# Optimization experiments

Measured on AMD Instinct MI355X. Metric: run time of the kernel, lower is better.

## Reference

```python
import jax, jax.numpy as jnp
import numpy as np

CR = 4; D = 768; H = 12; DH = 64; L = 3; I = 3072
W1S = 128  # one-sided sliding window = config.attention_window(256) // 2 (transformers convention)
MAXPOS = 7200; MLP = 512; NCLS = 3
EPS = 1e-12

def layer_norm(x, s, b):
    m = jnp.mean(x, -1, keepdims=True)
    v = jnp.var(x, -1, keepdims=True)
    return (x - m) * jax.lax.rsqrt(v + EPS) * s + b

def band_attention(q, k, v, w):
    # q,k,v: [B,H,S,dh]; each token attends to +-w neighbors (Longformer sliding chunks, no global tokens)
    B, Hh, S, dh = q.shape
    nc = S // w
    qc = q.reshape(B, Hh, nc, w, dh)
    kp = jnp.pad(k, ((0, 0), (0, 0), (w, w), (0, 0)))
    vp = jnp.pad(v, ((0, 0), (0, 0), (w, w), (0, 0)))
    idx = jnp.arange(nc)[:, None] * w + jnp.arange(3 * w)[None, :]          # [nc, 3w]
    kc = kp[:, :, idx]                                                      # [B,H,nc,3w,dh]
    vc = vp[:, :, idx]
    scores = jnp.einsum('bhcqd,bhckd->bhcqk', qc, kc) / np.float32(np.sqrt(dh))
    rel = jnp.arange(3 * w)[None, :] - w - jnp.arange(w)[:, None]           # [w,3w] key_pos - query_pos
    kpos = jnp.arange(nc)[:, None, None] * w + jnp.arange(3 * w)[None, None, :] - w
    mask = (jnp.abs(rel)[None] <= w) & (kpos >= 0) & (kpos < S)             # [nc,w,3w]
    scores = jnp.where(mask[None, None], scores, jnp.float32(-1e9))
    probs = jax.nn.softmax(scores, axis=-1)
    out = jnp.einsum('bhcqk,bhckd->bhcqd', probs, vc)
    return out.reshape(B, Hh, S, dh)

def forward(x, proj_w, proj_b, pos_emb, tok_emb, emb_ln_s, emb_ln_b,
            wq, bq, wk, bk, wv, bv, wo, bo, ln1_s, ln1_b,
            wi, bi, wo2, bo2, ln2_s, ln2_b,
            pool_w, pool_b, head_ln_s, head_ln_b, head_w1, head_b1, head_w2, head_b2):
    n, c, t, wd, hh = x.shape
    tc, sc = t // CR, wd // CR
    # torch unfold(dim, size, step) with size==step == contiguous block reshape
    xr = x[:, :, :tc * CR].reshape(n, c, CR, tc, CR, sc, CR, sc)
    xr = xr.transpose(0, 1, 2, 4, 6, 3, 5, 7)            # n,c,cr_t,cr_w,cr_h,tc,sc,sc
    xr = xr.reshape(n, c, CR ** 3, tc * sc * sc)
    xr = xr.transpose(0, 3, 2, 1).reshape(n, tc * sc * sc, CR ** 3 * c)
    h = xr @ proj_w + proj_b                             # [B,S,D]
    B, S = h.shape[0], h.shape[1]
    pos_ids = jnp.arange(S) % (MAXPOS - 2)               # no padding: S is already a multiple of 2w
    h = h + pos_emb[pos_ids][None] + tok_emb[0][None, None]
    h = layer_norm(h, emb_ln_s, emb_ln_b)
    for l in range(L):
        q = (h @ wq[l] + bq[l]).reshape(B, S, H, DH).transpose(0, 2, 1, 3)
        k = (h @ wk[l] + bk[l]).reshape(B, S, H, DH).transpose(0, 2, 1, 3)
        v = (h @ wv[l] + bv[l]).reshape(B, S, H, DH).transpose(0, 2, 1, 3)
        a = band_attention(q, k, v, W1S).transpose(0, 2, 1, 3).reshape(B, S, D)
        h = layer_norm(h + a @ wo[l] + bo[l], ln1_s[l], ln1_b[l])
        f = jax.nn.gelu(h @ wi[l] + bi[l], approximate=False) @ wo2[l] + bo2[l]
        h = layer_norm(h + f, ln2_s[l], ln2_b[l])
    pooled = jnp.tanh(h[:, 0] @ pool_w + pool_b)         # LongformerPooler on first token
    z = layer_norm(pooled, head_ln_s, head_ln_b)
    z = jax.nn.gelu(z @ head_w1 + head_b1, approximate=False)
    return z @ head_w2 + head_b2                         # [B, num_classes]

def setup_inputs() -> dict:
    key = jax.random.key(0)
    ks = iter(jax.random.split(key, 40))
    p = lambda *s: jax.random.normal(next(ks), s, jnp.float32) * 0.02
    d = {
        'x': jax.random.normal(next(ks), (8, 3, 64, 32, 32), jnp.float32),
        'position_ids': jnp.tile(jnp.arange(1024, dtype=jnp.int32)[None], (8, 1)),
        'proj_w': p(3 * CR ** 3, D), 'proj_b': p(D),
        'pos_emb': p(MAXPOS, D), 'tok_emb': p(2, D),
        'emb_ln_s': jnp.ones((D,), jnp.float32), 'emb_ln_b': jnp.zeros((D,), jnp.float32),
        'wq': p(L, D, D), 'bq': p(L, D), 'wk': p(L, D, D), 'bk': p(L, D),
        'wv': p(L, D, D), 'bv': p(L, D), 'wo': p(L, D, D), 'bo': p(L, D),
        'ln1_s': jnp.ones((L, D), jnp.float32), 'ln1_b': jnp.zeros((L, D), jnp.float32),
        'wi': p(L, D, I), 'bi': p(L, I), 'wo2': p(L, I, D), 'bo2': p(L, D),
        'ln2_s': jnp.ones((L, D), jnp.float32), 'ln2_b': jnp.zeros((L, D), jnp.float32),
        'pool_w': p(D, D), 'pool_b': p(D),
        'head_ln_s': jnp.ones((D,), jnp.float32), 'head_ln_b': jnp.zeros((D,), jnp.float32),
        'head_w1': p(D, MLP), 'head_b1': p(MLP),
        'head_w2': p(MLP, NCLS), 'head_b2': p(NCLS),
    }
    return d

def reference(x, position_ids, proj_w, proj_b, pos_emb, tok_emb, emb_ln_s, emb_ln_b,
              wq, bq, wk, bk, wv, bv, wo, bo, ln1_s, ln1_b,
              wi, bi, wo2, bo2, ln2_s, ln2_b,
              pool_w, pool_b, head_ln_s, head_ln_b, head_w1, head_b1, head_w2, head_b2):
    # position_ids is overwritten inside the spat_temp branch of the original forward (arange over cuboids)
    return forward(x, proj_w, proj_b, pos_emb, tok_emb, emb_ln_s, emb_ln_b,
                   wq, bq, wk, bk, wv, bv, wo, bo, ln1_s, ln1_b,
                   wi, bi, wo2, bo2, ln2_s, ln2_b,
                   pool_w, pool_b, head_ln_s, head_ln_b, head_w1, head_b1, head_w2, head_b2)
```

## Files before the change

kernel.cpp:

```cpp
#include <hip/hip_runtime.h>
#include <hip/hip_bf16.h>
#include <math.h>


typedef __attribute__((ext_vector_type(8))) short short8;
typedef __attribute__((ext_vector_type(4))) short short4v;
typedef __attribute__((ext_vector_type(4))) float floatx4;

__device__ __forceinline__ float gelu_exact(float x) {
    return 0.5f * x * (1.f + erff(x * 0.70710678118654752440f));
}

__device__ __forceinline__ short bfs(float x) {
    __hip_bfloat16 h = __float2bfloat16(x);
    short s;
    __builtin_memcpy(&s, &h, 2);
    return s;
}

__device__ __forceinline__ float bf2f(short s) {
    unsigned u = ((unsigned)(unsigned short)s) << 16;
    float f;
    __builtin_memcpy(&f, &u, 4);
    return f;
}

#define GLOAD_LDS16(g, l) __builtin_amdgcn_global_load_lds( \
    (const __attribute__((address_space(1))) void*)(g),     \
    (__attribute__((address_space(3))) void*)(l), 16, 0, 0)

__global__ __launch_bounds__(256) void transpose_bf16(
    const float* __restrict__ W, __hip_bfloat16* __restrict__ Wt,
    int K, int N, long inLS, long outLS)
{
    __shared__ float tile[32][33];
    int l = blockIdx.z;
    const float* Wl = W + (long)l * inLS;
    __hip_bfloat16* Wtl = Wt + (long)l * outLS;
    int lx = threadIdx.x & 31, ly = threadIdx.x >> 5;
    int kb = blockIdx.y * 32, nb = blockIdx.x * 32;
    #pragma unroll
    for (int r = 0; r < 32; r += 8)
        tile[ly + r][lx] = Wl[(long)(kb + ly + r) * N + nb + lx];
    __syncthreads();
    #pragma unroll
    for (int r = 0; r < 32; r += 8)
        Wtl[(long)(nb + ly + r) * K + kb + lx] = __float2bfloat16(tile[lx][ly + r]);
}

__global__ void pack_qkv_bias(const float* __restrict__ bq,
                              const float* __restrict__ bk,
                              const float* __restrict__ bv,
                              float* __restrict__ out)
{
    int l = blockIdx.x, tid = threadIdx.x;
    out[l * 2304 + tid]        = bq[l * 768 + tid];
    out[l * 2304 + 768 + tid]  = bk[l * 768 + tid];
    out[l * 2304 + 1536 + tid] = bv[l * 768 + tid];
}

__global__ __launch_bounds__(192) void gather_x(
    const float* __restrict__ x, __hip_bfloat16* __restrict__ xr)
{
    int tok = blockIdx.x;
    int b = tok >> 10, s = tok & 1023;
    int tci = s >> 6, sci = (s >> 3) & 7, scj = s & 7;
    int f = threadIdx.x;
    int ch  = f % 3;
    int crc = f / 3;
    int cr1 = crc >> 4, cr2 = (crc >> 2) & 3, cr3 = crc & 3;
    float v = x[(((b * 3 + ch) * 64) + cr1 * 16 + tci) * 1024 +
                (cr2 * 8 + sci) * 32 + cr3 * 8 + scj];
    xr[(long)tok * 192 + f] = __float2bfloat16(v);
}

template<int ACT>
__global__ __launch_bounds__(256) void mfma_gemm(
    const __hip_bfloat16* __restrict__ A, const __hip_bfloat16* __restrict__ Bt,
    const float* __restrict__ bias, __hip_bfloat16* __restrict__ C,
    int M, int N, int K)
{
    __shared__ short lds_raw[8704];
    __hip_bfloat16* As = (__hip_bfloat16*)lds_raw;
    __hip_bfloat16* Bs = As + 4096;
    int tid  = threadIdx.x;
    int wave = tid >> 6, lane = tid & 63;
    int L = blockIdx.x;
    long m0 = (long)(L & 63) * 128, n0 = (long)(L >> 6) * 128;
    int wr = wave >> 1, wc = wave & 1;
    floatx4 acc[4][4] = {};

    int srow = (wave * 128 + lane) >> 2;
    int sch  = (lane & 3) ^ ((lane >> 3) & 3);
    const __hip_bfloat16* Ag = A  + (m0 + srow) * K + sch * 8;
    const __hip_bfloat16* Bg = Bt + (n0 + srow) * K + sch * 8;
    __hip_bfloat16* AsW = &As[wave * 128 * 8];
    __hip_bfloat16* BsW = &Bs[wave * 128 * 8];
    int lm = lane & 15, lg = lane >> 4;
    int lk8 = ((lg ^ ((lm >> 1) & 3))) * 8;

    for (int k0 = 0; k0 < K; k0 += 32) {
        GLOAD_LDS16(Ag + k0,          AsW);
        GLOAD_LDS16(Ag + 16 * K + k0, AsW + 64 * 8);
        GLOAD_LDS16(Bg + k0,          BsW);
        GLOAD_LDS16(Bg + 16 * K + k0, BsW + 64 * 8);
        __syncthreads();
        short8 af[4], bf[4];
        #pragma unroll
        for (int mi = 0; mi < 4; mi++)
            af[mi] = *(const short8*)&As[(wr * 64 + mi * 16 + lm) * 32 + lk8];
        #pragma unroll
        for (int ni = 0; ni < 4; ni++)
            bf[ni] = *(const short8*)&Bs[(wc * 64 + ni * 16 + lm) * 32 + lk8];
        #pragma unroll
        for (int mi = 0; mi < 4; mi++)
            #pragma unroll
            for (int ni = 0; ni < 4; ni++)
                acc[mi][ni] = __builtin_amdgcn_mfma_f32_16x16x32_bf16(
                    af[mi], bf[ni], acc[mi][ni], 0, 0, 0);
        __syncthreads();
    }

    float bvv[4];
    #pragma unroll
    for (int ni = 0; ni < 4; ni++)
        bvv[ni] = bias[n0 + wc * 64 + ni * 16 + lm];
    int erow = tid >> 4;
    int ecol = (tid & 15) * 8;
    #pragma unroll
    for (int p = 0; p < 2; p++) {
        if (wr == p) {
            #pragma unroll
            for (int mi = 0; mi < 4; mi++)
                #pragma unroll
                for (int ni = 0; ni < 4; ni++)
                    #pragma unroll
                    for (int j = 0; j < 4; j++) {
                        float o = acc[mi][ni][j] + bvv[ni];
                        if (ACT == 1) o = gelu_exact(o);
                        lds_raw[(mi * 16 + lg * 4 + j) * 136 +
                                wc * 64 + ni * 16 + lm] = bfs(o);
                    }
        }
        __syncthreads();
        #pragma unroll
        for (int rr = 0; rr < 4; rr++) {
            int r = erow + rr * 16;
            short8 v = *(const short8*)&lds_raw[r * 136 + ecol];
            *(short8*)&C[(m0 + p * 64 + r) * N + n0 + ecol] = v;
        }
        __syncthreads();
    }
}

__global__ __launch_bounds__(256) void pos_ln_kernel(
    const __hip_bfloat16* __restrict__ t, const float* __restrict__ pos_emb,
    const float* __restrict__ tok_emb, const float* __restrict__ ln_s,
    const float* __restrict__ ln_b, float* __restrict__ h,
    __hip_bfloat16* __restrict__ hbf)
{
    int tok = blockIdx.x;
    int s = tok & 1023;
    int tid = threadIdx.x;
    __shared__ float red[8];
    const __hip_bfloat16* trow = &t[(long)tok * 768];
    int d0 = tid, d1 = tid + 256, d2 = tid + 512;
    float a0 = __bfloat162float(trow[d0]) + pos_emb[s * 768 + d0] + tok_emb[d0];
    float a1 = __bfloat162float(trow[d1]) + pos_emb[s * 768 + d1] + tok_emb[d1];
    float a2 = __bfloat162float(trow[d2]) + pos_emb[s * 768 + d2] + tok_emb[d2];
    float sum = a0 + a1 + a2;
    float sumsq = a0 * a0 + a1 * a1 + a2 * a2;
    #pragma unroll
    for (int off = 32; off; off >>= 1) {
        sum   += __shfl_down(sum, off, 64);
        sumsq += __shfl_down(sumsq, off, 64);
    }
    if ((tid & 63) == 0) { red[tid >> 6] = sum; red[4 + (tid >> 6)] = sumsq; }
    __syncthreads();
    sum   = red[0] + red[1] + red[2] + red[3];
    sumsq = red[4] + red[5] + red[6] + red[7];
    float mean = sum * (1.f / 768.f);
    float var  = sumsq * (1.f / 768.f) - mean * mean;
    float rs   = rsqrtf(var + 1e-12f);
    float* hrow = &h[(long)tok * 768];
    __hip_bfloat16* brow = &hbf[(long)tok * 768];
    float o0 = (a0 - mean) * rs * ln_s[d0] + ln_b[d0];
    float o1 = (a1 - mean) * rs * ln_s[d1] + ln_b[d1];
    float o2 = (a2 - mean) * rs * ln_s[d2] + ln_b[d2];
    hrow[d0] = o0; hrow[d1] = o1; hrow[d2] = o2;
    brow[d0] = __float2bfloat16(o0);
    brow[d1] = __float2bfloat16(o1);
    brow[d2] = __float2bfloat16(o2);
}

__global__ __launch_bounds__(256) void attn_kernel(
    const __hip_bfloat16* __restrict__ QKV, __hip_bfloat16* __restrict__ Ob)
{
    __shared__ __hip_bfloat16 KV[128 * 72];
    __shared__ __hip_bfloat16 Pl[4][32 * 136];
    __shared__ float alpha_s[4][32];
    __shared__ float l_s[4][32];

    int blk = blockIdx.x;
    int ci = blk & 7, hh = (blk >> 3) % 12, b = blk / 96;
    int tid = threadIdx.x, w = tid >> 6, lane = tid & 63;
    int lm = lane & 15, lg = lane >> 4;
    __hip_bfloat16* Pw = &Pl[w][0];

    short8 qf[2][2];
    #pragma unroll
    for (int nt = 0; nt < 2; nt++) {
        int q = ci * 128 + w * 32 + nt * 16 + lm;
        const __hip_bfloat16* qp = &QKV[((long)(b * 1024 + q)) * 2304 + hh * 64];
        #pragma unroll
        for (int ks = 0; ks < 2; ks++)
            qf[nt][ks] = *(const short8*)(qp + ks * 32 + lg * 8);
    }

    floatx4 accO[2][4] = {};
    float m_run[2] = {-1e30f, -1e30f};
    float l_run[2] = {0.f, 0.f};

    for (int tt = 0; tt < 3; tt++) {
        __syncthreads();
        #pragma unroll
        for (int i = 0; i < 4; i++) {
            int e = tid + i * 256;
            int jj = e >> 3, dd = (e & 7) * 8;
            int kpos = ci * 128 + tt * 128 + jj - 128;
            short8 kv = {};
            if (kpos >= 0 && kpos < 1024)
                kv = *(const short8*)&QKV[((long)(b * 1024 + kpos)) * 2304 + 768 + hh * 64 + dd];
            *(short8*)&KV[jj * 72 + dd] = kv;
        }
        __syncthreads();

        floatx4 accS[8][2] = {};
        #pragma unroll
        for (int ks = 0; ks < 2; ks++)
            #pragma unroll
            for (int mt = 0; mt < 8; mt++) {
                short8 kf = *(const short8*)&KV[(mt * 16 + lm) * 72 + ks * 32 + lg * 8];
                accS[mt][0] = __builtin_amdgcn_mfma_f32_16x16x32_bf16(kf, qf[0][ks], accS[mt][0], 0, 0, 0);
                accS[mt][1] = __builtin_amdgcn_mfma_f32_16x16x32_bf16(kf, qf[1][ks], accS[mt][1], 0, 0, 0);
            }

        float tmax[2] = {-1e30f, -1e30f};
        #pragma unroll
        for (int nt = 0; nt < 2; nt++) {
            int r = w * 32 + nt * 16 + lm;
            #pragma unroll
            for (int mt = 0; mt < 8; mt++)
                #pragma unroll
                for (int j = 0; j < 4; j++) {
                    int jrel = tt * 128 + mt * 16 + lg * 4 + j;
                    int kpos = ci * 128 + jrel - 128;
                    bool valid = (jrel >= r) && (jrel <= r + 256) &&
                                 (kpos >= 0) && (kpos < 1024);
                    float s = valid ? accS[mt][nt][j] * 0.125f : -1e9f;
                    accS[mt][nt][j] = s;
                    tmax[nt] = fmaxf(tmax[nt], s);
                }
            tmax[nt] = fmaxf(tmax[nt], __shfl_xor(tmax[nt], 16));
            tmax[nt] = fmaxf(tmax[nt], __shfl_xor(tmax[nt], 32));
        }

        float al[2];
        #pragma unroll
        for (int nt = 0; nt < 2; nt++) {
            float mnew = fmaxf(m_run[nt], tmax[nt]);
            al[nt] = __expf(m_run[nt] - mnew);
            m_run[nt] = mnew;
            float ts = 0.f;
            #pragma unroll
            for (int mt = 0; mt < 8; mt++) {
                short4v pp;
                #pragma unroll
                for (int j = 0; j < 4; j++) {
                    float p = __expf(accS[mt][nt][j] - mnew);
                    ts += p;
                    pp[j] = bfs(p);
                }
                *(short4v*)&Pw[(nt * 16 + lm) * 136 + mt * 16 + lg * 4] = pp;
            }
            ts += __shfl_xor(ts, 16);
            ts += __shfl_xor(ts, 32);
            l_run[nt] = l_run[nt] * al[nt] + ts;
        }
        if (lg < 2) alpha_s[w][lg * 16 + lm] = al[lg];

        __syncthreads();
        #pragma unroll
        for (int i = 0; i < 4; i++) {
            int e = tid + i * 256;
            int jj = e >> 3, dd = (e & 7) * 8;
            int kpos = ci * 128 + tt * 128 + jj - 128;
            short8 vv = {};
            if (kpos >= 0 && kpos < 1024)
                vv = *(const short8*)&QKV[((long)(b * 1024 + kpos)) * 2304 + 1536 + hh * 64 + dd];
            short* kvs = (short*)KV;
            #pragma unroll
            for (int m2 = 0; m2 < 8; m2++)
                kvs[(dd + m2) * 136 + jj] = vv[m2];
        }
        __syncthreads();

        #pragma unroll
        for (int mo = 0; mo < 2; mo++)
            #pragma unroll
            for (int j = 0; j < 4; j++) {
                float a = alpha_s[w][mo * 16 + lg * 4 + j];
                #pragma unroll
                for (int nd = 0; nd < 4; nd++)
                    accO[mo][nd][j] *= a;
            }

        #pragma unroll
        for (int kk = 0; kk < 4; kk++) {
            short8 pf[2], vf[4];
            #pragma unroll
            for (int mo = 0; mo < 2; mo++)
                pf[mo] = *(const short8*)&Pw[(mo * 16 + lm) * 136 + kk * 32 + lg * 8];
            #pragma unroll
            for (int nd = 0; nd < 4; nd++)
                vf[nd] = *(const short8*)&KV[(nd * 16 + lm) * 136 + kk * 32 + lg * 8];
            #pragma unroll
            for (int mo = 0; mo < 2; mo++)
                #pragma unroll
                for (int nd = 0; nd < 4; nd++)
                    accO[mo][nd] = __builtin_amdgcn_mfma_f32_16x16x32_bf16(
                        pf[mo], vf[nd], accO[mo][nd], 0, 0, 0);
        }
    }

    if (lg < 2) l_s[w][lg * 16 + lm] = l_run[lg];
    #pragma unroll
    for (int mo = 0; mo < 2; mo++)
        #pragma unroll
        for (int j = 0; j < 4; j++) {
            int qr = mo * 16 + lg * 4 + j;
            float rl = 1.f / l_s[w][qr];
            int q  = w * 32 + qr;
            long base = ((long)(b * 1024 + ci * 128 + q)) * 768 + hh * 64;
            #pragma unroll
            for (int nd = 0; nd < 4; nd++)
                Ob[base + nd * 16 + lm] = __float2bfloat16(accO[mo][nd][j] * rl);
        }
}

__global__ __launch_bounds__(256) void add_ln_kernel(
    float* __restrict__ h, const __hip_bfloat16* __restrict__ t,
    const float* __restrict__ ln_s, const float* __restrict__ ln_b,
    __hip_bfloat16* __restrict__ hbf)
{
    int tok = blockIdx.x;
    int tid = threadIdx.x;
    __shared__ float red[8];
    float* hrow = &h[(long)tok * 768];
    const __hip_bfloat16* trow = &t[(long)tok * 768];
    int d0 = tid, d1 = tid + 256, d2 = tid + 512;
    float a0 = hrow[d0] + __bfloat162float(trow[d0]);
    float a1 = hrow[d1] + __bfloat162float(trow[d1]);
    float a2 = hrow[d2] + __bfloat162float(trow[d2]);
    float sum = a0 + a1 + a2;
    float sumsq = a0 * a0 + a1 * a1 + a2 * a2;
    #pragma unroll
    for (int off = 32; off; off >>= 1) {
        sum   += __shfl_down(sum, off, 64);
        sumsq += __shfl_down(sumsq, off, 64);
    }
    if ((tid & 63) == 0) { red[tid >> 6] = sum; red[4 + (tid >> 6)] = sumsq; }
    __syncthreads();
    sum   = red[0] + red[1] + red[2] + red[3];
    sumsq = red[4] + red[5] + red[6] + red[7];
    float mean = sum * (1.f / 768.f);
    float var  = sumsq * (1.f / 768.f) - mean * mean;
    float rs   = rsqrtf(var + 1e-12f);
    __hip_bfloat16* brow = &hbf[(long)tok * 768];
    float o0 = (a0 - mean) * rs * ln_s[d0] + ln_b[d0];
    float o1 = (a1 - mean) * rs * ln_s[d1] + ln_b[d1];
    float o2 = (a2 - mean) * rs * ln_s[d2] + ln_b[d2];
    hrow[d0] = o0; hrow[d1] = o1; hrow[d2] = o2;
    brow[d0] = __float2bfloat16(o0);
    brow[d1] = __float2bfloat16(o1);
    brow[d2] = __float2bfloat16(o2);
}

__global__ __launch_bounds__(256) void pool_split(
    const __hip_bfloat16* __restrict__ hbf, const __hip_bfloat16* __restrict__ pool_wt,
    const float* __restrict__ pool_b, float* __restrict__ pooled)
{
    int g = blockIdx.x * 256 + threadIdx.x;
    int out = g >> 3, t8 = g & 7;
    int b = out / 768, d = out - b * 768;
    const __hip_bfloat16* hr = hbf + (long)b * 1024 * 768;
    const __hip_bfloat16* wr = pool_wt + (long)d * 768;
    float acc = 0.f;
    #pragma unroll
    for (int kk = 0; kk < 96; kk += 8) {
        int k = t8 * 96 + kk;
        short8 hv = *(const short8*)&hr[k];
        short8 wv = *(const short8*)&wr[k];
        #pragma unroll
        for (int j = 0; j < 8; j++) acc += bf2f(hv[j]) * bf2f(wv[j]);
    }
    acc += __shfl_down(acc, 4, 64);
    acc += __shfl_down(acc, 2, 64);
    acc += __shfl_down(acc, 1, 64);
    if (t8 == 0) pooled[out] = tanhf(acc + pool_b[d]);
}

__global__ __launch_bounds__(256) void ln_z_kernel(
    const float* __restrict__ pooled, const float* __restrict__ hln_s,
    const float* __restrict__ hln_b, __hip_bfloat16* __restrict__ zbf)
{
    int b = blockIdx.x, tid = threadIdx.x;
    __shared__ float red[8];
    const float* pr = &pooled[b * 768];
    float p0 = pr[tid], p1 = pr[tid + 256], p2 = pr[tid + 512];
    float sum = p0 + p1 + p2;
    float sumsq = p0 * p0 + p1 * p1 + p2 * p2;
    #pragma unroll
    for (int off = 32; off; off >>= 1) {
        sum   += __shfl_down(sum, off, 64);
        sumsq += __shfl_down(sumsq, off, 64);
    }
    if ((tid & 63) == 0) { red[tid >> 6] = sum; red[4 + (tid >> 6)] = sumsq; }
    __syncthreads();
    sum   = red[0] + red[1] + red[2] + red[3];
    sumsq = red[4] + red[5] + red[6] + red[7];
    float mean = sum * (1.f / 768.f);
    float var  = sumsq * (1.f / 768.f) - mean * mean;
    float rs   = rsqrtf(var + 1e-12f);
    zbf[b * 768 + tid]       = __float2bfloat16((p0 - mean) * rs * hln_s[tid]       + hln_b[tid]);
    zbf[b * 768 + tid + 256] = __float2bfloat16((p1 - mean) * rs * hln_s[tid + 256] + hln_b[tid + 256]);
    zbf[b * 768 + tid + 512] = __float2bfloat16((p2 - mean) * rs * hln_s[tid + 512] + hln_b[tid + 512]);
}

__global__ __launch_bounds__(256) void mlp_split(
    const __hip_bfloat16* __restrict__ zbf, const __hip_bfloat16* __restrict__ w1t,
    const float* __restrict__ b1, float* __restrict__ z1)
{
    int g = blockIdx.x * 256 + threadIdx.x;
    int out = g >> 3, t8 = g & 7;
    int b = out >> 9, d = out & 511;
    const __hip_bfloat16* zr = zbf + b * 768;
    const __hip_bfloat16* wr = w1t + (long)d * 768;
    float acc = 0.f;
    #pragma unroll
    for (int kk = 0; kk < 96; kk += 8) {
        int k = t8 * 96 + kk;
        short8 zv = *(const short8*)&zr[k];
        short8 wv = *(const short8*)&wr[k];
        #pragma unroll
        for (int j = 0; j < 8; j++) acc += bf2f(zv[j]) * bf2f(wv[j]);
    }
    acc += __shfl_down(acc, 4, 64);
    acc += __shfl_down(acc, 2, 64);
    acc += __shfl_down(acc, 1, 64);
    if (t8 == 0) z1[out] = gelu_exact(acc + b1[d]);
}

__global__ __launch_bounds__(256) void head_final_kernel(
    const float* __restrict__ z1, const float* __restrict__ w2,
    const float* __restrict__ b2, float* __restrict__ out)
{
    int tid = threadIdx.x;
    int g = tid >> 3, t8 = tid & 7;
    if (g < 24) {
        int b = g / 3, o = g % 3;
        float acc = 0.f;
        for (int k = t8; k < 512; k += 8)
            acc += z1[b * 512 + k] * w2[k * 3 + o];
        acc += __shfl_down(acc, 4, 64);
        acc += __shfl_down(acc, 2, 64);
        acc += __shfl_down(acc, 1, 64);
        if (t8 == 0) out[b * 3 + o] = acc + b2[o];
    }
}

extern "C" void kernel_launch(void* const* d_in, const int* in_sizes, int n_in,
                              void* d_out, int out_size, void* d_ws, size_t ws_size,
                              hipStream_t stream) {
    const float* x       = (const float*)d_in[0];
    const float* proj_w  = (const float*)d_in[2];
    const float* proj_b  = (const float*)d_in[3];
    const float* pos_emb = (const float*)d_in[4];
    const float* tok_emb = (const float*)d_in[5];
    const float* eln_s   = (const float*)d_in[6];
    const float* eln_b   = (const float*)d_in[7];
    const float* wq      = (const float*)d_in[8];
    const float* bq      = (const float*)d_in[9];
    const float* wk      = (const float*)d_in[10];
    const float* bk      = (const float*)d_in[11];
    const float* wv      = (const float*)d_in[12];
    const float* bv      = (const float*)d_in[13];
    const float* wo      = (const float*)d_in[14];
    const float* bo      = (const float*)d_in[15];
    const float* ln1_s   = (const float*)d_in[16];
    const float* ln1_b   = (const float*)d_in[17];
    const float* wi      = (const float*)d_in[18];
    const float* bi      = (const float*)d_in[19];
    const float* wo2     = (const float*)d_in[20];
    const float* bo2     = (const float*)d_in[21];
    const float* ln2_s   = (const float*)d_in[22];
    const float* ln2_b   = (const float*)d_in[23];
    const float* pool_w  = (const float*)d_in[24];
    const float* pool_b  = (const float*)d_in[25];
    const float* hln_s   = (const float*)d_in[26];
    const float* hln_b   = (const float*)d_in[27];
    const float* hw1     = (const float*)d_in[28];
    const float* hb1     = (const float*)d_in[29];
    const float* hw2     = (const float*)d_in[30];
    const float* hb2     = (const float*)d_in[31];

    char* wp = (char*)d_ws;
    auto alloc = [&](size_t bytes) {
        char* p = wp; wp += (bytes + 255) & ~(size_t)255; return p;
    };
    float*          h       = (float*)alloc(8192ll * 768 * 4);
    __hip_bfloat16* qkv_bf  = (__hip_bfloat16*)alloc(8192ll * 2304 * 2);
    __hip_bfloat16* t_bf    = (__hip_bfloat16*)alloc(8192ll * 768 * 2);
    __hip_bfloat16* mlp_bf  = (__hip_bfloat16*)alloc(8192ll * 3072 * 2);
    __hip_bfloat16* h_bf    = (__hip_bfloat16*)alloc(8192ll * 768 * 2);
    __hip_bfloat16* a_bf    = (__hip_bfloat16*)alloc(8192ll * 768 * 2);
    __hip_bfloat16* qkvw_t  = (__hip_bfloat16*)alloc(3ll * 2304 * 768 * 2);
    __hip_bfloat16* wo_t    = (__hip_bfloat16*)alloc(3ll * 768 * 768 * 2);
    __hip_bfloat16* wi_t    = (__hip_bfloat16*)alloc(3ll * 3072 * 768 * 2);
    __hip_bfloat16* wo2_t   = (__hip_bfloat16*)alloc(3ll * 768 * 3072 * 2);
    float*          qkv_b   = (float*)alloc(3ll * 2304 * 4);
    __hip_bfloat16* xr_bf   = (__hip_bfloat16*)alloc(8192ll * 192 * 2);
    __hip_bfloat16* projw_t = (__hip_bfloat16*)alloc(768ll * 192 * 2);
    __hip_bfloat16* poolw_t = (__hip_bfloat16*)alloc(768ll * 768 * 2);
    __hip_bfloat16* w1_t    = (__hip_bfloat16*)alloc(512ll * 768 * 2);
    float*          pooled  = (float*)alloc(8ll * 768 * 4);
    __hip_bfloat16* z_bf    = (__hip_bfloat16*)alloc(8ll * 768 * 2);
    float*          z1      = (float*)alloc(8ll * 512 * 4);

    transpose_bf16<<<dim3(24, 24, 3), 256, 0, stream>>>(wq, qkvw_t,               768, 768,  768ll * 768,  2304ll * 768);
    transpose_bf16<<<dim3(24, 24, 3), 256, 0, stream>>>(wk, qkvw_t + 768 * 768,   768, 768,  768ll * 768,  2304ll * 768);
    transpose_bf16<<<dim3(24, 24, 3), 256, 0, stream>>>(wv, qkvw_t + 1536 * 768,  768, 768,  768ll * 768,  2304ll * 768);
    transpose_bf16<<<dim3(24, 24, 3), 256, 0, stream>>>(wo, wo_t,                 768, 768,  768ll * 768,  768ll * 768);
    transpose_bf16<<<dim3(96, 24, 3), 256, 0, stream>>>(wi, wi_t,                 768, 3072, 768ll * 3072, 3072ll * 768);
    transpose_bf16<<<dim3(24, 96, 3), 256, 0, stream>>>(wo2, wo2_t,               3072, 768, 3072ll * 768, 768ll * 3072);
    transpose_bf16<<<dim3(24, 6, 1),  256, 0, stream>>>(proj_w, projw_t,          192, 768,  0, 0);
    transpose_bf16<<<dim3(24, 24, 1), 256, 0, stream>>>(pool_w, poolw_t,          768, 768,  0, 0);
    transpose_bf16<<<dim3(16, 24, 1), 256, 0, stream>>>(hw1, w1_t,                768, 512,  0, 0);
    pack_qkv_bias<<<3, 768, 0, stream>>>(bq, bk, bv, qkv_b);

    gather_x<<<8192, 192, 0, stream>>>(x, xr_bf);
    mfma_gemm<0><<<6 * 64, 256, 0, stream>>>(
        xr_bf, projw_t, proj_b, t_bf, 8192, 768, 192);
    pos_ln_kernel<<<8192, 256, 0, stream>>>(t_bf, pos_emb, tok_emb, eln_s, eln_b, h, h_bf);

    for (int l = 0; l < 3; l++) {
        mfma_gemm<0><<<18 * 64, 256, 0, stream>>>(
            h_bf, qkvw_t + (long)l * 2304 * 768, qkv_b + l * 2304, qkv_bf,
            8192, 2304, 768);
        attn_kernel<<<768, 256, 0, stream>>>(qkv_bf, a_bf);
        mfma_gemm<0><<<6 * 64, 256, 0, stream>>>(
            a_bf, wo_t + (long)l * 768 * 768, bo + l * 768, t_bf,
            8192, 768, 768);
        add_ln_kernel<<<8192, 256, 0, stream>>>(h, t_bf, ln1_s + l * 768, ln1_b + l * 768, h_bf);
        mfma_gemm<1><<<24 * 64, 256, 0, stream>>>(
            h_bf, wi_t + (long)l * 3072 * 768, bi + l * 3072, mlp_bf,
            8192, 3072, 768);
        mfma_gemm<0><<<6 * 64, 256, 0, stream>>>(
            mlp_bf, wo2_t + (long)l * 768 * 3072, bo2 + l * 768, t_bf,
            8192, 768, 3072);
        add_ln_kernel<<<8192, 256, 0, stream>>>(h, t_bf, ln2_s + l * 768, ln2_b + l * 768, h_bf);
    }

    pool_split<<<192, 256, 0, stream>>>(h_bf, poolw_t, pool_b, pooled);
    ln_z_kernel<<<8, 256, 0, stream>>>(pooled, hln_s, hln_b, z_bf);
    mlp_split<<<128, 256, 0, stream>>>(z_bf, w1_t, hb1, z1);
    head_final_kernel<<<1, 256, 0, stream>>>(z1, hw2, hb2, (float*)d_out);
}
```

Measured before the change: 1.195 ms.

## Double-buffer GEMM LDS loads, vectorize LayerNorm kernels, approximate GELU erf

The GEMM now uses two LDS buffers and prefetches the next K-slice with global_load_lds while the current one is being consumed. This drops one barrier per iteration and overlaps global loads with MFMA work, at the cost of twice the LDS footprint, which may lower occupancy. The LayerNorm kernels switch to 192 threads that each handle 4 contiguous elements through float4 and short4 vector loads and stores. GELU's erff is replaced with an Abramowitz-Stegun polynomial using __expf, which is cheaper but less accurate.

```diff
diff --git a/kernel.cpp b/kernel.cpp
--- a/kernel.cpp
+++ b/kernel.cpp
@@ -8,7 +8,12 @@
 typedef __attribute__((ext_vector_type(4))) float floatx4;
 
 __device__ __forceinline__ float gelu_exact(float x) {
-    return 0.5f * x * (1.f + erff(x * 0.70710678118654752440f));
+    float ax = fabsf(x) * 0.70710678118654752440f;
+    float t  = 1.f / (1.f + 0.3275911f * ax);
+    float y  = t * (0.254829592f + t * (-0.284496736f + t * (1.421413741f +
+               t * (-1.453152027f + t * 1.061405429f))));
+    float erfv = copysignf(1.f - y * __expf(-ax * ax), x);
+    return 0.5f * x * (1.f + erfv);
 }
 
 __device__ __forceinline__ short bfs(float x) {
@@ -80,9 +85,9 @@
     const float* __restrict__ bias, __hip_bfloat16* __restrict__ C,
     int M, int N, int K)
 {
-    __shared__ short lds_raw[8704];
+    __shared__ short lds_raw[16384];
     __hip_bfloat16* As = (__hip_bfloat16*)lds_raw;
-    __hip_bfloat16* Bs = As + 4096;
+    __hip_bfloat16* Bs = As + 8192;
     int tid  = threadIdx.x;
     int wave = tid >> 6, lane = tid & 63;
     int L = blockIdx.x;
@@ -94,32 +99,40 @@
     int sch  = (lane & 3) ^ ((lane >> 3) & 3);
     const __hip_bfloat16* Ag = A  + (m0 + srow) * K + sch * 8;
     const __hip_bfloat16* Bg = Bt + (n0 + srow) * K + sch * 8;
-    __hip_bfloat16* AsW = &As[wave * 128 * 8];
-    __hip_bfloat16* BsW = &Bs[wave * 128 * 8];
     int lm = lane & 15, lg = lane >> 4;
     int lk8 = ((lg ^ ((lm >> 1) & 3))) * 8;
 
-    for (int k0 = 0; k0 < K; k0 += 32) {
-        GLOAD_LDS16(Ag + k0,          AsW);
-        GLOAD_LDS16(Ag + 16 * K + k0, AsW + 64 * 8);
-        GLOAD_LDS16(Bg + k0,          BsW);
-        GLOAD_LDS16(Bg + 16 * K + k0, BsW + 64 * 8);
-        __syncthreads();
-        short8 af[4], bf[4];
+    auto stage = [&](int buf, int k0) {
+        __hip_bfloat16* a = As + buf * 4096 + wave * 1024;
+        __hip_bfloat16* b = Bs + buf * 4096 + wave * 1024;
+        GLOAD_LDS16(Ag + k0,          a);
+        GLOAD_LDS16(Ag + 16 * K + k0, a + 512);
+        GLOAD_LDS16(Bg + k0,          b);
+        GLOAD_LDS16(Bg + 16 * K + k0, b + 512);
+    };
+
+    stage(0, 0);
+    int buf = 0;
+    for (int k0 = 0; k0 < K; k0 += 32, buf ^= 1) {
+        __syncthreads();
+        if (k0 + 32 < K) stage(buf ^ 1, k0 + 32);
+        const __hip_bfloat16* Ab = As + buf * 4096;
+        const __hip_bfloat16* Bb = Bs + buf * 4096;
+        short8 af[4], bf4[4];
         #pragma unroll
         for (int mi = 0; mi < 4; mi++)
-            af[mi] = *(const short8*)&As[(wr * 64 + mi * 16 + lm) * 32 + lk8];
+            af[mi] = *(const short8*)&Ab[(wr * 64 + mi * 16 + lm) * 32 + lk8];
         #pragma unroll
         for (int ni = 0; ni < 4; ni++)
-            bf[ni] = *(const short8*)&Bs[(wc * 64 + ni * 16 + lm) * 32 + lk8];
+            bf4[ni] = *(const short8*)&Bb[(wc * 64 + ni * 16 + lm) * 32 + lk8];
         #pragma unroll
         for (int mi = 0; mi < 4; mi++)
             #pragma unroll
             for (int ni = 0; ni < 4; ni++)
                 acc[mi][ni] = __builtin_amdgcn_mfma_f32_16x16x32_bf16(
-                    af[mi], bf[ni], acc[mi][ni], 0, 0, 0);
-        __syncthreads();
-    }
+                    af[mi], bf4[ni], acc[mi][ni], 0, 0, 0);
+    }
+    __syncthreads();
 
     float bvv[4];
     #pragma unroll
@@ -153,7 +166,7 @@
     }
 }
 
-__global__ __launch_bounds__(256) void pos_ln_kernel(
+__global__ __launch_bounds__(192) void pos_ln_kernel(
     const __hip_bfloat16* __restrict__ t, const float* __restrict__ pos_emb,
     const float* __restrict__ tok_emb, const float* __restrict__ ln_s,
     const float* __restrict__ ln_b, float* __restrict__ h,
@@ -162,35 +175,37 @@
     int tok = blockIdx.x;
     int s = tok & 1023;
     int tid = threadIdx.x;
-    __shared__ float red[8];
-    const __hip_bfloat16* trow = &t[(long)tok * 768];
-    int d0 = tid, d1 = tid + 256, d2 = tid + 512;
-    float a0 = __bfloat162float(trow[d0]) + pos_emb[s * 768 + d0] + tok_emb[d0];
-    float a1 = __bfloat162float(trow[d1]) + pos_emb[s * 768 + d1] + tok_emb[d1];
-    float a2 = __bfloat162float(trow[d2]) + pos_emb[s * 768 + d2] + tok_emb[d2];
-    float sum = a0 + a1 + a2;
-    float sumsq = a0 * a0 + a1 * a1 + a2 * a2;
+    int d = tid * 4;
+    __shared__ float red[6];
+    short4v tv = *(const short4v*)&t[(long)tok * 768 + d];
+    float4 pv = *(const float4*)&pos_emb[s * 768 + d];
+    float4 kv = *(const float4*)&tok_emb[d];
+    float a[4] = { bf2f(tv[0]) + pv.x + kv.x, bf2f(tv[1]) + pv.y + kv.y,
+                   bf2f(tv[2]) + pv.z + kv.z, bf2f(tv[3]) + pv.w + kv.w };
+    float sum = a[0] + a[1] + a[2] + a[3];
+    float sumsq = a[0]*a[0] + a[1]*a[1] + a[2]*a[2] + a[3]*a[3];
     #pragma unroll
     for (int off = 32; off; off >>= 1) {
         sum   += __shfl_down(sum, off, 64);
         sumsq += __shfl_down(sumsq, off, 64);
     }
-    if ((tid & 63) == 0) { red[tid >> 6] = sum; red[4 + (tid >> 6)] = sumsq; }
+    if ((tid & 63) == 0) { red[tid >> 6] = sum; red[3 + (tid >> 6)] = sumsq; }
     __syncthreads();
-    sum   = red[0] + red[1] + red[2] + red[3];
-    sumsq = red[4] + red[5] + red[6] + red[7];
+    sum   = red[0] + red[1] + red[2];
+    sumsq = red[3] + red[4] + red[5];
     float mean = sum * (1.f / 768.f);
     float var  = sumsq * (1.f / 768.f) - mean * mean;
     float rs   = rsqrtf(var + 1e-12f);
-    float* hrow = &h[(long)tok * 768];
-    __hip_bfloat16* brow = &hbf[(long)tok * 768];
-    float o0 = (a0 - mean) * rs * ln_s[d0] + ln_b[d0];
-    float o1 = (a1 - mean) * rs * ln_s[d1] + ln_b[d1];
-    float o2 = (a2 - mean) * rs * ln_s[d2] + ln_b[d2];
-    hrow[d0] = o0; hrow[d1] = o1; hrow[d2] = o2;
-    brow[d0] = __float2bfloat16(o0);
-    brow[d1] = __float2bfloat16(o1);
-    brow[d2] = __float2bfloat16(o2);
+    float4 sv = *(const float4*)&ln_s[d];
+    float4 bv = *(const float4*)&ln_b[d];
+    float4 o;
+    o.x = (a[0] - mean) * rs * sv.x + bv.x;
+    o.y = (a[1] - mean) * rs * sv.y + bv.y;
+    o.z = (a[2] - mean) * rs * sv.z + bv.z;
+    o.w = (a[3] - mean) * rs * sv.w + bv.w;
+    *(float4*)&h[(long)tok * 768 + d] = o;
+    short4v ob = { bfs(o.x), bfs(o.y), bfs(o.z), bfs(o.w) };
+    *(short4v*)&hbf[(long)tok * 768 + d] = ob;
 }
 
 __global__ __launch_bounds__(256) void attn_kernel(
@@ -348,42 +363,44 @@
         }
 }
 
-__global__ __launch_bounds__(256) void add_ln_kernel(
+__global__ __launch_bounds__(192) void add_ln_kernel(
     float* __restrict__ h, const __hip_bfloat16* __restrict__ t,
     const float* __restrict__ ln_s, const float* __restrict__ ln_b,
     __hip_bfloat16* __restrict__ hbf)
 {
     int tok = blockIdx.x;
     int tid = threadIdx.x;
-    __shared__ float red[8];
+    int d = tid * 4;
+    __shared__ float red[6];
     float* hrow = &h[(long)tok * 768];
-    const __hip_bfloat16* trow = &t[(long)tok * 768];
-    int d0 = tid, d1 = tid + 256, d2 = tid + 512;
-    float a0 = hrow[d0] + __bfloat162float(trow[d0]);
-    float a1 = hrow[d1] + __bfloat162float(trow[d1]);
-    float a2 = hrow[d2] + __bfloat162float(trow[d2]);
-    float sum = a0 + a1 + a2;
-    float sumsq = a0 * a0 + a1 * a1 + a2 * a2;
+    float4 hv = *(const float4*)&hrow[d];
+    short4v tv = *(const short4v*)&t[(long)tok * 768 + d];
+    float a[4] = { hv.x + bf2f(tv[0]), hv.y + bf2f(tv[1]),
+                   hv.z + bf2f(tv[2]), hv.w + bf2f(tv[3]) };
+    float sum = a[0] + a[1] + a[2] + a[3];
+    float sumsq = a[0]*a[0] + a[1]*a[1] + a[2]*a[2] + a[3]*a[3];
     #pragma unroll
     for (int off = 32; off; off >>= 1) {
         sum   += __shfl_down(sum, off, 64);
         sumsq += __shfl_down(sumsq, off, 64);
     }
-    if ((tid & 63) == 0) { red[tid >> 6] = sum; red[4 + (tid >> 6)] = sumsq; }
+    if ((tid & 63) == 0) { red[tid >> 6] = sum; red[3 + (tid >> 6)] = sumsq; }
     __syncthreads();
-    sum   = red[0] + red[1] + red[2] + red[3];
-    sumsq = red[4] + red[5] + red[6] + red[7];
+    sum   = red[0] + red[1] + red[2];
+    sumsq = red[3] + red[4] + red[5];
     float mean = sum * (1.f / 768.f);
     float var  = sumsq * (1.f / 768.f) - mean * mean;
     float rs   = rsqrtf(var + 1e-12f);
-    __hip_bfloat16* brow = &hbf[(long)tok * 768];
-    float o0 = (a0 - mean) * rs * ln_s[d0] + ln_b[d0];
-    float o1 = (a1 - mean) * rs * ln_s[d1] + ln_b[d1];
-    float o2 = (a2 - mean) * rs * ln_s[d2] + ln_b[d2];
-    hrow[d0] = o0; hrow[d1] = o1; hrow[d2] = o2;
-    brow[d0] = __float2bfloat16(o0);
-    brow[d1] = __float2bfloat16(o1);
-    brow[d2] = __float2bfloat16(o2);
+    float4 sv = *(const float4*)&ln_s[d];
+    float4 bv = *(const float4*)&ln_b[d];
+    float4 o;
+    o.x = (a[0] - mean) * rs * sv.x + bv.x;
+    o.y = (a[1] - mean) * rs * sv.y + bv.y;
+    o.z = (a[2] - mean) * rs * sv.z + bv.z;
+    o.w = (a[3] - mean) * rs * sv.w + bv.w;
+    *(float4*)&hrow[d] = o;
+    short4v ob = { bfs(o.x), bfs(o.y), bfs(o.z), bfs(o.w) };
+    *(short4v*)&hbf[(long)tok * 768 + d] = ob;
 }
 
 __global__ __launch_bounds__(256) void pool_split(
@@ -551,7 +568,7 @@
     gather_x<<<8192, 192, 0, stream>>>(x, xr_bf);
     mfma_gemm<0><<<6 * 64, 256, 0, stream>>>(
         xr_bf, projw_t, proj_b, t_bf, 8192, 768, 192);
-    pos_ln_kernel<<<8192, 256, 0, stream>>>(t_bf, pos_emb, tok_emb, eln_s, eln_b, h, h_bf);
+    pos_ln_kernel<<<8192, 192, 0, stream>>>(t_bf, pos_emb, tok_emb, eln_s, eln_b, h, h_bf);
 
     for (int l = 0; l < 3; l++) {
         mfma_gemm<0><<<18 * 64, 256, 0, stream>>>(
@@ -561,14 +578,14 @@
         mfma_gemm<0><<<6 * 64, 256, 0, stream>>>(
             a_bf, wo_t + (long)l * 768 * 768, bo + l * 768, t_bf,
             8192, 768, 768);
-        add_ln_kernel<<<8192, 256, 0, stream>>>(h, t_bf, ln1_s + l * 768, ln1_b + l * 768, h_bf);
+        add_ln_kernel<<<8192, 192, 0, stream>>>(h, t_bf, ln1_s + l * 768, ln1_b + l * 768, h_bf);
         mfma_gemm<1><<<24 * 64, 256, 0, stream>>>(
             h_bf, wi_t + (long)l * 3072 * 768, bi + l * 3072, mlp_bf,
             8192, 3072, 768);
         mfma_gemm<0><<<6 * 64, 256, 0, stream>>>(
             mlp_bf, wo2_t + (long)l * 768 * 3072, bo2 + l * 768, t_bf,
             8192, 768, 3072);
-        add_ln_kernel<<<8192, 256, 0, stream>>>(h, t_bf, ln2_s + l * 768, ln2_b + l * 768, h_bf);
+        add_ln_kernel<<<8192, 192, 0, stream>>>(h, t_bf, ln2_s + l * 768, ln2_b + l * 768, h_bf);
     }
 
     pool_split<<<192, 256, 0, stream>>>(h_bf, poolw_t, pool_b, pooled);
```

After: 1.091 ms. 8.7% less time.
